# Optimization experiments

Hardware: AMD Instinct MI355X
Metric: run time of the kernel (lower is better)

The kernel has to match this reference:

```python
import jax, jax.numpy as jnp
import numpy as np

METRIC = (1.0, 1.0, 1.0, 1.0, -1.0)  # Cl(4,1) signature
N_HEADS = 8
EPS = 1e-6


def _cayley():
    # Cayley table C[a, b, k]: e_a * e_b = sum_k C[a,b,k] e_k, blades indexed by bitmask over 5 generators.
    C = np.zeros((32, 32, 32), dtype=np.float32)
    for a in range(32):
        for b in range(32):
            s = 0
            t = a >> 1
            while t:
                s += bin(t & b).count('1')
                t >>= 1
            sign = -1.0 if (s & 1) else 1.0
            for i in range(5):
                if (a & b) >> i & 1:
                    sign *= METRIC[i]
            C[a, b, a ^ b] = sign
    return C

_C_NP = _cayley()
GP_MAP = jnp.asarray(_C_NP)  # (32,32,32)
SIG = jnp.asarray(_C_NP[np.arange(32), np.arange(32), 0])  # blade square signs, (32,)


def normalize_cl41(x):
    # normalize each multivector (last-dim 32 blades) to unit RMS
    return x / jnp.sqrt(jnp.mean(x * x, axis=-1, keepdims=True) + EPS)


def versor_linear(x, W):
    # x: (B,S,I,32), W: (O,I,32); out_k = sum_{i,j,l} W[o,i,j] C[j,l,k] x[b,s,i,l]
    O, I, _ = W.shape
    W_op = jnp.einsum('oij,jlk->oilk', W, GP_MAP)  # (O,I,32,32)
    W_mat = W_op.transpose(1, 2, 0, 3).reshape(I * 32, O * 32)
    B, S = x.shape[0], x.shape[1]
    out = (x.reshape(B, S, I * 32) @ W_mat).reshape(B, S, O, 32)
    return normalize_cl41(out)


def versor_attention(x, Wq, Wk, Wv, Wo, lam):
    B, S, D, _ = x.shape
    H = N_HEADS
    hd = D // H

    def split_heads(t):  # (B,S,D,32) -> (B,H,S,hd,32)
        return t.reshape(B, S, H, hd, 32).transpose(0, 2, 1, 3, 4)

    q = split_heads(versor_linear(x, Wq))
    k = split_heads(versor_linear(x, Wk))
    v = split_heads(versor_linear(x, Wv))

    q_flat = (q * SIG).reshape(B, H, S, hd * 32)  # signature-weighted
    k_flat = k.reshape(B, H, S, hd * 32)

    scalar = jnp.einsum('bhsd,bhtd->bhst', q_flat, k_flat)
    scale = 1.0 / jnp.sqrt(jnp.asarray(hd, x.dtype))
    score = scalar * scale

    # torque term: sqrt(relu(|q|^2 |k|^2 - (q.k)^2) + eps) / sqrt(hd)
    q_norm_sq = jnp.sum(q_flat * q_flat, axis=-1)[..., :, None]  # (B,H,S,1)
    k_norm_sq = jnp.sum(k_flat * k_flat, axis=-1)[..., None, :]  # (B,H,1,S)
    torque = jnp.sqrt(jax.nn.relu(q_norm_sq * k_norm_sq - scalar * scalar) + EPS) * scale
    score = score + lam * torque

    probs = jax.nn.softmax(score, axis=-1)
    out = jnp.einsum('bhst,bhtdl->bhsdl', probs, v)  # (B,H,S,hd,32)
    out = out.transpose(0, 2, 1, 3, 4).reshape(B, S, D, 32)
    return versor_linear(out, Wo)


def setup_inputs() -> dict:
    key = jax.random.key(0)
    ks = jax.random.split(key, 5)
    B, S, D = 2, 1024, 128
    std = (2.0 / (D * 32)) ** 0.5  # Versor init
    x = jax.random.normal(ks[0], (B, S, D, 32), jnp.float32)
    Wq = jax.random.normal(ks[1], (D, D, 32), jnp.float32) * std
    Wk = jax.random.normal(ks[2], (D, D, 32), jnp.float32) * std
    Wv = jax.random.normal(ks[3], (D, D, 32), jnp.float32) * std
    Wo = jax.random.normal(ks[4], (D, D, 32), jnp.float32) * std
    attn_lambda = jnp.float32(0.1)
    return {'x': x, 'Wq': Wq, 'Wk': Wk, 'Wv': Wv, 'Wo': Wo, 'attn_lambda': attn_lambda}


def reference(x, Wq, Wk, Wv, Wo, attn_lambda):
    return versor_attention(x, Wq, Wk, Wv, Wo, attn_lambda)
```

## Files before the change

kernel.cpp:

```cpp
#include <hip/hip_runtime.h>
#include <stdint.h>

typedef __attribute__((ext_vector_type(4))) float    f32x4;
typedef __attribute__((ext_vector_type(8))) short    s16x8;
typedef __attribute__((ext_vector_type(4))) short    s16x4;
typedef __attribute__((ext_vector_type(8))) _Float16 f16x8;

#define DEV __device__ __forceinline__

DEV float blade_sign(int a, int b){
    int s = 0, t = a >> 1;
    while (t){ s += __popc(t & b); t >>= 1; }
    float sg = (s & 1) ? -1.0f : 1.0f;
    return ((a & b) & 16) ? -sg : sg;
}
DEV short f2h(float v){
    _Float16 h = (_Float16)v;
    return __builtin_bit_cast(short, h);
}
DEV float h2f(short b){
    return (float)__builtin_bit_cast(_Float16, b);
}
DEV void wait_vm(int n){
    if (n == 8)      asm volatile("s_waitcnt vmcnt(8)" ::: "memory");
    else if (n == 6) asm volatile("s_waitcnt vmcnt(6)" ::: "memory");
    else if (n == 4) asm volatile("s_waitcnt vmcnt(4)" ::: "memory");
    else             asm volatile("s_waitcnt vmcnt(0)" ::: "memory");
}

__global__ __launch_bounds__(256) void cast_f32_f16(const float* __restrict__ in,
                                                    short* __restrict__ out){
    const size_t idx = (size_t)blockIdx.x * 256 + threadIdx.x;
    const float4* p = reinterpret_cast<const float4*>(in) + idx * 2;
    float4 a = p[0], b = p[1];
    s16x8 o;
    o[0]=f2h(a.x); o[1]=f2h(a.y); o[2]=f2h(a.z); o[3]=f2h(a.w);
    o[4]=f2h(b.x); o[5]=f2h(b.y); o[6]=f2h(b.z); o[7]=f2h(b.w);
    *reinterpret_cast<s16x8*>(out + idx * 8) = o;
}

DEV void build_wmat_body(const float* __restrict__ W, short* __restrict__ WmT,
                         int idx){
    const int n  = idx >> 9;
    const int kg = idx & 511;
    const int o = n >> 5, kb = n & 31;
    const int i = kg >> 2, l0 = (kg & 3) * 8;
    const float* wrow = W + (size_t)(o * 128 + i) * 32;
    s16x8 v;
    #pragma unroll
    for (int e = 0; e < 8; ++e){
        const int l = l0 + e, j = kb ^ l;
        v[e] = f2h(wrow[j] * blade_sign(j, l));
    }
    *reinterpret_cast<s16x8*>(WmT + (size_t)n * 4096 + kg * 8) = v;
}

__global__ __launch_bounds__(256) void build_wmat(const float* __restrict__ W,
                                                  short* __restrict__ WmT){
    build_wmat_body(W, WmT, blockIdx.x * 256 + threadIdx.x);
}

__global__ __launch_bounds__(256) void build_wmat3(const float* __restrict__ Wq,
                                                   const float* __restrict__ Wk,
                                                   const float* __restrict__ Wv,
                                                   short* __restrict__ WmT3){
    const int w = blockIdx.y;
    const float* W = (w == 0) ? Wq : ((w == 1) ? Wk : Wv);
    build_wmat_body(W, WmT3 + (size_t)w * 4096 * 4096,
                    blockIdx.x * 256 + threadIdx.x);
}

__global__ __launch_bounds__(256) void row_norms(const short* __restrict__ Q,
                                                 const short* __restrict__ Kq,
                                                 float* __restrict__ Nq,
                                                 float* __restrict__ Nk){
    const int row  = blockIdx.x * 4 + (threadIdx.x >> 6);
    const int lane = threadIdx.x & 63;
    const int b = row >> 13, h = (row >> 10) & 7, s = row & 1023;
    const size_t off = ((size_t)(b * 1024 + s)) * 4096 + h * 512 + lane * 8;
    s16x8 a = *reinterpret_cast<const s16x8*>(Q + off);
    s16x8 c = *reinterpret_cast<const s16x8*>(Kq + off);
    float sq = 0.f, sk = 0.f;
    #pragma unroll
    for (int e = 0; e < 8; ++e){
        float fa = h2f(a[e]); sq = fmaf(fa, fa, sq);
        float fc = h2f(c[e]); sk = fmaf(fc, fc, sk);
    }
    #pragma unroll
    for (int m = 1; m < 64; m <<= 1){
        sq += __shfl_xor(sq, m);
        sk += __shfl_xor(sk, m);
    }
    if (lane == 0){ Nq[row] = sq; Nk[row] = sk; }
}

__global__ __launch_bounds__(256) void softmax_rows(float* __restrict__ Sc){
    const int row  = blockIdx.x * 4 + (threadIdx.x >> 6);
    const int lane = threadIdx.x & 63;
    float* p = Sc + (size_t)row * 1024;
    float v[16];
    float mx = -3.0e38f;
    #pragma unroll
    for (int j = 0; j < 16; ++j){ v[j] = p[lane + j * 64]; mx = fmaxf(mx, v[j]); }
    #pragma unroll
    for (int m = 1; m < 64; m <<= 1) mx = fmaxf(mx, __shfl_xor(mx, m));
    float sum = 0.f;
    #pragma unroll
    for (int j = 0; j < 16; ++j){ v[j] = __expf(v[j] - mx); sum += v[j]; }
    #pragma unroll
    for (int m = 1; m < 64; m <<= 1) sum += __shfl_xor(sum, m);
    const float inv = 1.0f / sum;
    short* pb = reinterpret_cast<short*>(p);
    #pragma unroll
    for (int j = 0; j < 16; ++j) pb[lane + j * 64] = f2h(v[j] * inv);
}

#define GLOAD_LDS(gp, lp) \
    __builtin_amdgcn_global_load_lds( \
        (const __attribute__((address_space(1))) void*)(const void*)(gp), \
        (__attribute__((address_space(3))) void*)(void*)(lp), 16, 0, 0)

#define QKV_STAGE(BUF, T)                                                       \
  {                                                                             \
    const int sb = (BUF) * 12288;                                               \
    GLOAD_LDS(gA0 + (size_t)(T) * 32, lds + sb + dA + 0 * 512);                 \
    GLOAD_LDS(gA1 + (size_t)(T) * 32, lds + sb + dA + 1 * 512);                 \
    GLOAD_LDS(gA2 + (size_t)(T) * 32, lds + sb + dA + 2 * 512);                 \
    GLOAD_LDS(gA3 + (size_t)(T) * 32, lds + sb + dA + 3 * 512);                 \
    GLOAD_LDS(gB0 + (size_t)(T) * 32, lds + sb + dB + 0 * 512);                 \
    GLOAD_LDS(gB1 + (size_t)(T) * 32, lds + sb + dB + 1 * 512);                 \
  }

__global__ __launch_bounds__(256, 3) void versor_gemm_qkv4(
    const short* __restrict__ Xf,
    const short* __restrict__ WmT3,
    short* __restrict__ OQ,
    short* __restrict__ OK,
    short* __restrict__ OV)
{
    __shared__ short lds[2 * 12288];

    const int tid  = threadIdx.x;
    const int lane = tid & 63;
    const int wid  = tid >> 6;
    const int wm   = wid >> 1;
    const int wn   = wid & 1;

    const int wg  = blockIdx.x + blockIdx.y * 96;
    const int xcd = wg & 7;
    const int u   = wg >> 3;
    const int bm  = u & 7;
    const int bn  = xcd * 12 + (u >> 3);
    const int row0 = bm * 256;
    const int col0 = bn * 128;
    const int lda = 4096, ldb = 4096;

    const int jsw = ((lane & 3) ^ ((lane >> 3) & 3)) * 8;
    const short* gA0 = Xf + (size_t)(row0 + wid * 64 + (lane >> 2)) * lda + jsw;
    const short* gA1 = gA0 + (size_t)16 * lda;
    const short* gA2 = gA0 + (size_t)32 * lda;
    const short* gA3 = gA0 + (size_t)48 * lda;
    const short* gB0 = WmT3 + (size_t)(col0 + wid * 32 + (lane >> 2)) * ldb + jsw;
    const short* gB1 = gB0 + (size_t)16 * ldb;
    const int dA = wid * 4 * 512;
    const int dB = 8192 + wid * 2 * 512;

    const int swz = ((lane >> 4) ^ (((lane & 15) >> 1) & 3)) * 8;
    const int ard = (wm * 128 + (lane & 15)) * 32 + swz;
    const int brd = 8192 + (wn * 64 + (lane & 15)) * 32 + swz;

    f32x4 acc[8][4];
    #pragma unroll
    for (int i = 0; i < 8; ++i)
        #pragma unroll
        for (int j = 0; j < 4; ++j)
            acc[i][j] = (f32x4){0.f, 0.f, 0.f, 0.f};

    const int NT = 4096 >> 5;

    QKV_STAGE(0, 0)
    QKV_STAGE(1, 1)

    for (int t = 0; t < NT; ++t){
        if (t + 1 < NT) wait_vm(6);
        else            wait_vm(0);
        __builtin_amdgcn_s_barrier();
        asm volatile("" ::: "memory");
        __builtin_amdgcn_sched_barrier(0);

        const int bb = (t & 1) * 12288;
        f16x8 av[4], bv[4];
        #pragma unroll
        for (int i = 0; i < 4; ++i){
            av[i] = *reinterpret_cast<const f16x8*>(lds + bb + ard + i * 512);
            bv[i] = *reinterpret_cast<const f16x8*>(lds + bb + brd + i * 512);
        }
        __builtin_amdgcn_s_setprio(1);
        #pragma unroll
        for (int mi = 0; mi < 4; ++mi)
            #pragma unroll
            for (int ni = 0; ni < 4; ++ni)
                acc[mi][ni] = __builtin_amdgcn_mfma_f32_16x16x32_f16(
                    av[mi], bv[ni], acc[mi][ni], 0, 0, 0);
        __builtin_amdgcn_s_setprio(0);

        f16x8 aw[4];
        #pragma unroll
        for (int i = 0; i < 4; ++i)
            aw[i] = *reinterpret_cast<const f16x8*>(lds + bb + ard + (4 + i) * 512);
        __builtin_amdgcn_s_setprio(1);
        #pragma unroll
        for (int mi = 0; mi < 4; ++mi)
            #pragma unroll
            for (int ni = 0; ni < 4; ++ni)
                acc[4 + mi][ni] = __builtin_amdgcn_mfma_f32_16x16x32_f16(
                    aw[mi], bv[ni], acc[4 + mi][ni], 0, 0, 0);
        __builtin_amdgcn_s_setprio(0);

        __builtin_amdgcn_s_barrier();
        asm volatile("" ::: "memory");
        __builtin_amdgcn_sched_barrier(0);
        if (t + 2 < NT)
            QKV_STAGE(t & 1, t + 2)
    }

    const int rb = row0 + wm * 128 + (lane >> 4) * 4;

    #pragma unroll
    for (int mi = 0; mi < 8; ++mi){
        #pragma unroll
        for (int g = 0; g < 2; ++g){
            f32x4 a0 = acc[mi][2 * g], a1 = acc[mi][2 * g + 1];
            f32x4 ss = a0 * a0 + a1 * a1;
            #pragma unroll
            for (int m = 1; m < 16; m <<= 1){
                ss.x += __shfl_xor(ss.x, m);
                ss.y += __shfl_xor(ss.y, m);
                ss.z += __shfl_xor(ss.z, m);
                ss.w += __shfl_xor(ss.w, m);
            }
            f32x4 inv;
            inv.x = 1.0f / sqrtf(ss.x * 0.03125f + 1e-6f);
            inv.y = 1.0f / sqrtf(ss.y * 0.03125f + 1e-6f);
            inv.z = 1.0f / sqrtf(ss.z * 0.03125f + 1e-6f);
            inv.w = 1.0f / sqrtf(ss.w * 0.03125f + 1e-6f);
            acc[mi][2 * g]     = a0 * inv;
            acc[mi][2 * g + 1] = a1 * inv;
        }
    }

    const int zsel = col0 >> 12;
    const int cbm  = (col0 & 4095) + wn * 64 + (lane & 15);
    if (zsel == 0){
        const float sg0 = blade_sign(lane & 15, lane & 15);
        const float sg1 = blade_sign(16 | (lane & 15), 16 | (lane & 15));
        #pragma unroll
        for (int mi = 0; mi < 8; ++mi)
            #pragma unroll
            for (int ni = 0; ni < 4; ++ni){
                const f32x4 v = acc[mi][ni] * ((ni & 1) ? sg1 : sg0);
                #pragma unroll
                for (int j = 0; j < 4; ++j)
                    OQ[(size_t)(rb + mi * 16 + j) * 4096 + (cbm + ni * 16)] = f2h(v[j]);
            }
    } else if (zsel == 1){
        #pragma unroll
        for (int mi = 0; mi < 8; ++mi)
            #pragma unroll
            for (int ni = 0; ni < 4; ++ni)
                #pragma unroll
                for (int j = 0; j < 4; ++j)
                    OK[(size_t)(rb + mi * 16 + j) * 4096 + (cbm + ni * 16)] = f2h(acc[mi][ni][j]);
    } else {
        #pragma unroll
        for (int mi = 0; mi < 8; ++mi){
            const int r = rb + mi * 16;
            const int b = r >> 10, tt = r & 1023;
            #pragma unroll
            for (int ni = 0; ni < 4; ++ni){
                const int c = cbm + ni * 16;
                const int h = c >> 9, f = c & 511;
                s16x4 pv;
                #pragma unroll
                for (int j = 0; j < 4; ++j) pv[j] = f2h(acc[mi][ni][j]);
                *reinterpret_cast<s16x4*>(OV + ((size_t)((b * 8 + h) * 512 + f)) * 1024 + tt) = pv;
            }
        }
    }
}

#define R3_TILE(T, WN, PF)                                                      \
  {                                                                             \
    const int bb = cur * 8192;                                                  \
    wait_vm(WN);                                                                \
    __builtin_amdgcn_s_barrier();                                               \
    asm volatile("" ::: "memory");                                              \
    __builtin_amdgcn_sched_barrier(0);                                          \
    const int sb = stg * 8192;                                                  \
    if (PF){                                                                    \
        GLOAD_LDS(gA0 + (size_t)((T) + 2) * 32, lds + sb + dA0);                \
        GLOAD_LDS(gA1 + (size_t)((T) + 2) * 32, lds + sb + dA1);                \
    }                                                                           \
    f16x8 av[4], bv[4];                                                         \
    _Pragma("unroll")                                                           \
    for (int i = 0; i < 4; ++i)                                                 \
        av[i] = *reinterpret_cast<const f16x8*>(lds + bb + ard + i * 512);      \
    bv[0] = *reinterpret_cast<const f16x8*>(lds + bb + brd + 0 * 512);          \
    bv[1] = *reinterpret_cast<const f16x8*>(lds + bb + brd + 1 * 512);          \
    __builtin_amdgcn_s_setprio(1);                                              \
    _Pragma("unroll")                                                           \
    for (int mi = 0; mi < 4; ++mi)                                              \
        _Pragma("unroll")                                                       \
        for (int ni = 0; ni < 2; ++ni)                                          \
            acc[mi][ni] = __builtin_amdgcn_mfma_f32_16x16x32_f16(               \
                av[mi], bv[ni], acc[mi][ni], 0, 0, 0);                          \
    __builtin_amdgcn_s_setprio(0);                                              \
    if (PF){                                                                    \
        GLOAD_LDS(gB0 + (size_t)((T) + 2) * 32, lds + sb + dB0);                \
        GLOAD_LDS(gB1 + (size_t)((T) + 2) * 32, lds + sb + dB1);                \
    }                                                                           \
    bv[2] = *reinterpret_cast<const f16x8*>(lds + bb + brd + 2 * 512);          \
    bv[3] = *reinterpret_cast<const f16x8*>(lds + bb + brd + 3 * 512);          \
    __builtin_amdgcn_s_setprio(1);                                              \
    _Pragma("unroll")                                                           \
    for (int mi = 0; mi < 4; ++mi)                                              \
        _Pragma("unroll")                                                       \
        for (int ni = 2; ni < 4; ++ni)                                          \
            acc[mi][ni] = __builtin_amdgcn_mfma_f32_16x16x32_f16(               \
                av[mi], bv[ni], acc[mi][ni], 0, 0, 0);                          \
    __builtin_amdgcn_s_setprio(0);                                              \
    cur = (cur == 2) ? 0 : cur + 1;                                             \
    stg = (stg == 2) ? 0 : stg + 1;                                             \
  }

template<int EPI, int CPX>
__global__ __launch_bounds__(256, 3) void versor_gemm_r3(
    const short* __restrict__ Abase, int lda,
    const short* __restrict__ Bbase, int ldb,
    int K, void* __restrict__ OutP)
{
    __shared__ short lds[3 * 8192];

    const int tid  = threadIdx.x;
    const int lane = tid & 63;
    const int wid  = tid >> 6;
    const int wr   = wid >> 1;
    const int wc   = wid & 1;
    const int z    = blockIdx.z;

    int bn, bm;
    if constexpr (CPX > 0){
        const int wg  = blockIdx.x + blockIdx.y * gridDim.x;
        const int xcd = wg & 7;
        const int u   = wg >> 3;
        bm = u & 15;
        bn = xcd * CPX + (u >> 4);
    } else {
        bn = blockIdx.x; bm = blockIdx.y;
    }

    const short* A = Abase;
    const short* B = Bbase;
    if constexpr (EPI == 5){
        A += (size_t)z * 1024 * 2048;
        B += (size_t)z * 512 * 1024;
    }
    const int row0 = bm * 128;
    const int col0 = bn * 128;

    const int jsw = ((lane & 3) ^ ((lane >> 3) & 3)) * 8;
    const short* gA0 = A + (size_t)(row0 + wid * 16 + (lane >> 2)) * lda + jsw;
    const short* gA1 = gA0 + (size_t)64 * lda;
    const short* gB0 = B + (size_t)(col0 + wid * 16 + (lane >> 2)) * ldb + jsw;
    const short* gB1 = gB0 + (size_t)64 * ldb;
    const int dA0 = wid * 512,        dA1 = 2048 + wid * 512;
    const int dB0 = 4096 + wid * 512, dB1 = 6144 + wid * 512;

    const int swz = ((lane >> 4) ^ (((lane & 15) >> 1) & 3)) * 8;
    const int ard = (wr * 64 + (lane & 15)) * 32 + swz;
    const int brd = 4096 + (wc * 64 + (lane & 15)) * 32 + swz;

    f32x4 acc[4][4];
    #pragma unroll
    for (int i = 0; i < 4; ++i)
        #pragma unroll
        for (int j = 0; j < 4; ++j)
            acc[i][j] = (f32x4){0.f, 0.f, 0.f, 0.f};

    const int NT = K >> 5;

    #pragma unroll
    for (int pt = 0; pt < 2; ++pt){
        const int sb = pt * 8192;
        GLOAD_LDS(gA0 + pt * 32, lds + sb + dA0);
        GLOAD_LDS(gA1 + pt * 32, lds + sb + dA1);
        GLOAD_LDS(gB0 + pt * 32, lds + sb + dB0);
        GLOAD_LDS(gB1 + pt * 32, lds + sb + dB1);
    }

    int cur = 0, stg = 2;
    for (int t = 0; t < NT - 1; ++t)
        R3_TILE(t, 4, (t + 2 < NT))
    R3_TILE(NT - 1, 0, false)

    const int rb = row0 + wr * 64 + (lane >> 4) * 4;
    const int cb = col0 + wc * 64 + (lane & 15);

    if constexpr (EPI == 3){
        #pragma unroll
        for (int mi = 0; mi < 4; ++mi){
            #pragma unroll
            for (int g = 0; g < 2; ++g){
                f32x4 a0 = acc[mi][2 * g], a1 = acc[mi][2 * g + 1];
                f32x4 ss = a0 * a0 + a1 * a1;
                #pragma unroll
                for (int m = 1; m < 16; m <<= 1){
                    ss.x += __shfl_xor(ss.x, m);
                    ss.y += __shfl_xor(ss.y, m);
                    ss.z += __shfl_xor(ss.z, m);
                    ss.w += __shfl_xor(ss.w, m);
                }
                f32x4 inv;
                inv.x = 1.0f / sqrtf(ss.x * 0.03125f + 1e-6f);
                inv.y = 1.0f / sqrtf(ss.y * 0.03125f + 1e-6f);
                inv.z = 1.0f / sqrtf(ss.z * 0.03125f + 1e-6f);
                inv.w = 1.0f / sqrtf(ss.w * 0.03125f + 1e-6f);
                acc[mi][2 * g]     = a0 * inv;
                acc[mi][2 * g + 1] = a1 * inv;
            }
        }
        float* Of = (float*)OutP;
        #pragma unroll
        for (int mi = 0; mi < 4; ++mi)
            #pragma unroll
            for (int ni = 0; ni < 4; ++ni)
                #pragma unroll
                for (int j = 0; j < 4; ++j)
                    Of[(size_t)(rb + mi * 16 + j) * 4096 + (cb + ni * 16)] = acc[mi][ni][j];
    }
    if constexpr (EPI == 5){
        short* Ob = (short*)OutP;
        const int b = z >> 3, h = z & 7;
        #pragma unroll
        for (int mi = 0; mi < 4; ++mi)
            #pragma unroll
            for (int ni = 0; ni < 4; ++ni)
                #pragma unroll
                for (int j = 0; j < 4; ++j)
                    Ob[(size_t)(b * 1024 + rb + mi * 16 + j) * 4096 + h * 512 + (cb + ni * 16)]
                        = f2h(acc[mi][ni][j]);
    }
}

#define SC_TILE(T, WN, PF)                                                      \
  {                                                                             \
    const int bb = ((T) & 3) * 16384;                                           \
    wait_vm(WN);                                                                \
    __builtin_amdgcn_s_barrier();                                               \
    asm volatile("" ::: "memory");                                              \
    __builtin_amdgcn_sched_barrier(0);                                          \
    if (PF){                                                                    \
        const int nb = (((T) + 3) & 3) * 16384;                                 \
        GLOAD_LDS(gA0 + (size_t)((T) + 3) * 32, lds + nb + dA0);                \
        GLOAD_LDS(gA1 + (size_t)((T) + 3) * 32, lds + nb + dA1);                \
    }                                                                           \
    f16x8 av[4], bv[4];                                                         \
    _Pragma("unroll")                                                           \
    for (int i = 0; i < 4; ++i){                                                \
        av[i] = *reinterpret_cast<const f16x8*>(lds + bb + ard + i * 512);      \
        bv[i] = *reinterpret_cast<const f16x8*>(lds + bb + brd + i * 512);      \
    }                                                                           \
    __builtin_amdgcn_s_setprio(1);                                              \
    _Pragma("unroll")                                                           \
    for (int mi = 0; mi < 4; ++mi)                                              \
        _Pragma("unroll")                                                       \
        for (int ni = 0; ni < 4; ++ni)                                          \
            acc[mi][ni] = __builtin_amdgcn_mfma_f32_16x16x32_f16(               \
                av[mi], bv[ni], acc[mi][ni], 0, 0, 0);                          \
    __builtin_amdgcn_s_setprio(0);                                              \
    if (PF){                                                                    \
        const int nb = (((T) + 3) & 3) * 16384;                                 \
        GLOAD_LDS(gB0 + (size_t)((T) + 3) * 32, lds + nb + dB0);                \
        GLOAD_LDS(gB1 + (size_t)((T) + 3) * 32, lds + nb + dB1);                \
    }                                                                           \
    f16x8 aw[4];                                                                \
    _Pragma("unroll")                                                           \
    for (int i = 0; i < 4; ++i)                                                 \
        aw[i] = *reinterpret_cast<const f16x8*>(lds + bb + ard + (4 + i) * 512);\
    __builtin_amdgcn_s_setprio(1);                                              \
    _Pragma("unroll")                                                           \
    for (int mi = 0; mi < 4; ++mi)                                              \
        _Pragma("unroll")                                                       \
        for (int ni = 0; ni < 4; ++ni)                                          \
            acc[4 + mi][ni] = __builtin_amdgcn_mfma_f32_16x16x32_f16(           \
                aw[mi], bv[ni], acc[4 + mi][ni], 0, 0, 0);                      \
    __builtin_amdgcn_s_setprio(0);                                              \
  }

__global__ __launch_bounds__(512, 2) void versor_gemm_sc(
    const short* __restrict__ Qbase, const short* __restrict__ Kbase,
    int K, float* __restrict__ OutP,
    const float* __restrict__ NqP, const float* __restrict__ NkP,
    const float* __restrict__ LamP)
{
    extern __shared__ short lds[];

    const int tid  = threadIdx.x;
    const int lane = tid & 63;
    const int wid  = tid >> 6;
    const int wm   = wid >> 2;
    const int wn   = wid & 3;
    const int z    = blockIdx.z;

    const int b = z >> 3, h = z & 7;
    const size_t off = (size_t)b * 1024 * 4096 + (size_t)h * 512;
    const short* A = Qbase + off;
    const short* B = Kbase + off;
    const int lda = 4096, ldb = 4096;
    const int row0 = blockIdx.y * 256;
    const int col0 = blockIdx.x * 256;

    const int jsw = ((lane & 3) ^ ((lane >> 3) & 3)) * 8;
    const short* gA0 = A + (size_t)(row0 + wid * 32 + (lane >> 2)) * lda + jsw;
    const short* gA1 = gA0 + (size_t)16 * lda;
    const short* gB0 = B + (size_t)(col0 + wid * 32 + (lane >> 2)) * ldb + jsw;
    const short* gB1 = gB0 + (size_t)16 * ldb;
    const int dA0 = wid * 1024, dA1 = dA0 + 512;
    const int dB0 = 8192 + wid * 1024, dB1 = dB0 + 512;

    const int swz = ((lane >> 4) ^ (((lane & 15) >> 1) & 3)) * 8;
    const int ard = (wm * 128 + (lane & 15)) * 32 + swz;
    const int brd = 8192 + (wn * 64 + (lane & 15)) * 32 + swz;

    f32x4 acc[8][4];
    #pragma unroll
    for (int i = 0; i < 8; ++i)
        #pragma unroll
        for (int j = 0; j < 4; ++j)
            acc[i][j] = (f32x4){0.f, 0.f, 0.f, 0.f};

    const int NT = K >> 5;

    #pragma unroll
    for (int pt = 0; pt < 3; ++pt){
        const int bb = pt * 16384;
        GLOAD_LDS(gA0 + pt * 32, lds + bb + dA0);
        GLOAD_LDS(gA1 + pt * 32, lds + bb + dA1);
        GLOAD_LDS(gB0 + pt * 32, lds + bb + dB0);
        GLOAD_LDS(gB1 + pt * 32, lds + bb + dB1);
    }

    for (int t = 0; t < NT - 2; ++t)
        SC_TILE(t, 8, (t + 3 < NT))
    SC_TILE(NT - 2, 4, false)
    SC_TILE(NT - 1, 0, false)

    const int rb = row0 + wm * 128 + (lane >> 4) * 4;
    const int cb = col0 + wn * 64 + (lane & 15);

    float* Of = OutP + (size_t)z * 1024 * 1024;
    const float lam = *LamP;
    const float* nq = NqP + z * 1024;
    const float* nk = NkP + z * 1024;
    #pragma unroll
    for (int mi = 0; mi < 8; ++mi)
        #pragma unroll
        for (int j = 0; j < 4; ++j){
            const int r = rb + mi * 16 + j;
            const float qn = nq[r];
            #pragma unroll
            for (int ni = 0; ni < 4; ++ni){
                const int c = cb + ni * 16;
                const float sc = acc[mi][ni][j];
                const float tq = sqrtf(fmaxf(qn * nk[c] - sc * sc, 0.0f) + 1e-6f);
                Of[(size_t)r * 1024 + c] = 0.25f * (sc + lam * tq);
            }
        }
}

extern "C" void kernel_launch(void* const* d_in, const int* in_sizes, int n_in,
                              void* d_out, int out_size, void* d_ws, size_t ws_size,
                              hipStream_t stream)
{
    (void)in_sizes; (void)n_in; (void)out_size; (void)ws_size;
    const float* x   = (const float*)d_in[0];
    const float* Wq  = (const float*)d_in[1];
    const float* Wk  = (const float*)d_in[2];
    const float* Wv  = (const float*)d_in[3];
    const float* Wo  = (const float*)d_in[4];
    const float* lam = (const float*)d_in[5];
    float* out = (float*)d_out;
    char*  ws  = (char*)d_ws;

    short* Xf   = (short*)(ws);
    short* WmT3 = (short*)(ws + (16u  << 20));
    short* Qf   = (short*)(ws + (112u << 20));
    short* Kf   = (short*)(ws + (128u << 20));
    short* Vt   = (short*)(ws + (144u << 20));
    float* Nq   = (float*)(ws + (160u << 20));
    float* Nk   = (float*)(ws + (160u << 20) + (64u << 10));
    float* Sc   = (float*)(ws + (16u  << 20));
    short* WmTo = (short*)(ws + (80u  << 20));
    short* Attn = Xf;

    const int SC_LDS = 131072;
    hipFuncSetAttribute(reinterpret_cast<const void*>(versor_gemm_sc),
                        hipFuncAttributeMaxDynamicSharedMemorySize, SC_LDS);

    dim3 blk(256), blk8(512);
    cast_f32_f16<<<4096, blk, 0, stream>>>(x, Xf);

    dim3 gw3(8192, 3);
    build_wmat3<<<gw3, blk, 0, stream>>>(Wq, Wk, Wv, WmT3);

    dim3 gqkv(96, 8, 1);
    versor_gemm_qkv4<<<gqkv, blk, 0, stream>>>(Xf, WmT3, Qf, Kf, Vt);

    row_norms<<<4096, blk, 0, stream>>>(Qf, Kf, Nq, Nk);

    build_wmat<<<8192, blk, 0, stream>>>(Wo, WmTo);

    dim3 gsc(4, 4, 16);
    versor_gemm_sc<<<gsc, blk8, SC_LDS, stream>>>(Qf, Kf, 512, Sc, Nq, Nk, lam);
    softmax_rows<<<4096, blk, 0, stream>>>(Sc);

    dim3 gpv(4, 8, 16);
    versor_gemm_r3<5, 0><<<gpv, blk, 0, stream>>>(
        (const short*)Sc, 2048, Vt, 1024, 1024, Attn);

    dim3 gfin(32, 16, 1);
    versor_gemm_r3<3, 4><<<gfin, blk, 0, stream>>>(
        Attn, 4096, WmTo, 4096, 4096, out);
}
```

Baseline: 528.5 us.

## Restructure QKV GEMM into 256x256 tiles with 8 waves and interleaved prefetch

Replaces the 256x128-tile, 4-wave QKV projection GEMM with a 256x256-tile, 8-wave kernel that uses 128 KB of dynamic LDS and a K-step of 64 split into two halves. Global-to-LDS prefetch of the next tile is spread across the MFMA phases with extra barriers, aiming for more operand reuse per loaded byte and better overlap of loads with math. The cost is one workgroup per CU (384 workgroups), more barriers per iteration, and less latency hiding from co-resident blocks.

```diff
diff --git a/kernel.cpp b/kernel.cpp
--- a/kernel.cpp
+++ b/kernel.cpp
@@ -120,54 +120,58 @@
         (const __attribute__((address_space(1))) void*)(const void*)(gp), \
         (__attribute__((address_space(3))) void*)(void*)(lp), 16, 0, 0)
 
-#define QKV_STAGE(BUF, T)                                                       \
-  {                                                                             \
-    const int sb = (BUF) * 12288;                                               \
-    GLOAD_LDS(gA0 + (size_t)(T) * 32, lds + sb + dA + 0 * 512);                 \
-    GLOAD_LDS(gA1 + (size_t)(T) * 32, lds + sb + dA + 1 * 512);                 \
-    GLOAD_LDS(gA2 + (size_t)(T) * 32, lds + sb + dA + 2 * 512);                 \
-    GLOAD_LDS(gA3 + (size_t)(T) * 32, lds + sb + dA + 3 * 512);                 \
-    GLOAD_LDS(gB0 + (size_t)(T) * 32, lds + sb + dB + 0 * 512);                 \
-    GLOAD_LDS(gB1 + (size_t)(T) * 32, lds + sb + dB + 1 * 512);                 \
-  }
-
-__global__ __launch_bounds__(256, 3) void versor_gemm_qkv4(
+#define Q7_ST_A(BUF, T, H)                                                      \
+  { short* d = lds + (BUF) * 32768 + (H) * 8192 + wid * 1024;                   \
+    const short* s = gA + (size_t)(T) * 64 + (H) * 32;                          \
+    GLOAD_LDS(s, d);                                                            \
+    GLOAD_LDS(s + (size_t)16 * 4096, d + 512); }
+
+#define Q7_ST_B(BUF, T, H)                                                      \
+  { short* d = lds + (BUF) * 32768 + 16384 + (H) * 8192 + wid * 1024;           \
+    const short* s = gB + (size_t)(T) * 64 + (H) * 32;                          \
+    GLOAD_LDS(s, d);                                                            \
+    GLOAD_LDS(s + (size_t)16 * 4096, d + 512); }
+
+#define Q7_MFMA8(MBASE, BK)                                                     \
+    __builtin_amdgcn_s_setprio(1);                                              \
+    _Pragma("unroll")                                                           \
+    for (int mi = 0; mi < 4; ++mi)                                              \
+        _Pragma("unroll")                                                       \
+        for (int ni = 0; ni < 4; ++ni)                                          \
+            acc[(MBASE) + mi][ni] = __builtin_amdgcn_mfma_f32_16x16x32_f16(     \
+                a[mi], BK[ni], acc[(MBASE) + mi][ni], 0, 0, 0);                 \
+    __builtin_amdgcn_s_setprio(0);
+
+__global__ __launch_bounds__(512, 1) void versor_gemm_qkv7(
     const short* __restrict__ Xf,
     const short* __restrict__ WmT3,
     short* __restrict__ OQ,
     short* __restrict__ OK,
     short* __restrict__ OV)
 {
-    __shared__ short lds[2 * 12288];
+    extern __shared__ short lds[];
 
     const int tid  = threadIdx.x;
     const int lane = tid & 63;
     const int wid  = tid >> 6;
-    const int wm   = wid >> 1;
-    const int wn   = wid & 1;
-
-    const int wg  = blockIdx.x + blockIdx.y * 96;
+    const int wm   = wid >> 2;
+    const int wn   = wid & 3;
+
+    const int wg  = blockIdx.x + blockIdx.y * 48;
     const int xcd = wg & 7;
     const int u   = wg >> 3;
     const int bm  = u & 7;
-    const int bn  = xcd * 12 + (u >> 3);
+    const int bn  = xcd * 6 + (u >> 3);
     const int row0 = bm * 256;
-    const int col0 = bn * 128;
-    const int lda = 4096, ldb = 4096;
+    const int col0 = bn * 256;
 
     const int jsw = ((lane & 3) ^ ((lane >> 3) & 3)) * 8;
-    const short* gA0 = Xf + (size_t)(row0 + wid * 64 + (lane >> 2)) * lda + jsw;
-    const short* gA1 = gA0 + (size_t)16 * lda;
-    const short* gA2 = gA0 + (size_t)32 * lda;
-    const short* gA3 = gA0 + (size_t)48 * lda;
-    const short* gB0 = WmT3 + (size_t)(col0 + wid * 32 + (lane >> 2)) * ldb + jsw;
-    const short* gB1 = gB0 + (size_t)16 * ldb;
-    const int dA = wid * 4 * 512;
-    const int dB = 8192 + wid * 2 * 512;
+    const short* gA = Xf   + (size_t)(row0 + wid * 32 + (lane >> 2)) * 4096 + jsw;
+    const short* gB = WmT3 + (size_t)(col0 + wid * 32 + (lane >> 2)) * 4096 + jsw;
 
     const int swz = ((lane >> 4) ^ (((lane & 15) >> 1) & 3)) * 8;
     const int ard = (wm * 128 + (lane & 15)) * 32 + swz;
-    const int brd = 8192 + (wn * 64 + (lane & 15)) * 32 + swz;
+    const int brd = (wn * 64 + (lane & 15)) * 32 + swz;
 
     f32x4 acc[8][4];
     #pragma unroll
@@ -176,52 +180,61 @@
         for (int j = 0; j < 4; ++j)
             acc[i][j] = (f32x4){0.f, 0.f, 0.f, 0.f};
 
-    const int NT = 4096 >> 5;
-
-    QKV_STAGE(0, 0)
-    QKV_STAGE(1, 1)
+    const int NT = 64;
+
+    Q7_ST_A(0, 0, 0)
+    Q7_ST_B(0, 0, 0)
+    Q7_ST_A(0, 0, 1)
+    Q7_ST_B(0, 0, 1)
 
     for (int t = 0; t < NT; ++t){
-        if (t + 1 < NT) wait_vm(6);
-        else            wait_vm(0);
+        const int bb = (t & 1) * 32768;
+        const int nbuf = (t + 1) & 1;
+        const bool pf = (t + 1 < NT);
+        f16x8 a[4], bk0[4], bk1[4];
+
+        wait_vm(4);
         __builtin_amdgcn_s_barrier();
         asm volatile("" ::: "memory");
         __builtin_amdgcn_sched_barrier(0);
-
-        const int bb = (t & 1) * 12288;
-        f16x8 av[4], bv[4];
-        #pragma unroll
-        for (int i = 0; i < 4; ++i){
-            av[i] = *reinterpret_cast<const f16x8*>(lds + bb + ard + i * 512);
-            bv[i] = *reinterpret_cast<const f16x8*>(lds + bb + brd + i * 512);
-        }
-        __builtin_amdgcn_s_setprio(1);
+        #pragma unroll
+        for (int ni = 0; ni < 4; ++ni)
+            bk0[ni] = *reinterpret_cast<const f16x8*>(lds + bb + 16384 + brd + ni * 512);
         #pragma unroll
         for (int mi = 0; mi < 4; ++mi)
-            #pragma unroll
-            for (int ni = 0; ni < 4; ++ni)
-                acc[mi][ni] = __builtin_amdgcn_mfma_f32_16x16x32_f16(
-                    av[mi], bv[ni], acc[mi][ni], 0, 0, 0);
-        __builtin_amdgcn_s_setprio(0);
-
-        f16x8 aw[4];
-        #pragma unroll
-        for (int i = 0; i < 4; ++i)
-            aw[i] = *reinterpret_cast<const f16x8*>(lds + bb + ard + (4 + i) * 512);
-        __builtin_amdgcn_s_setprio(1);
+            a[mi] = *reinterpret_cast<const f16x8*>(lds + bb + ard + mi * 512);
+        if (pf) Q7_ST_A(nbuf, t + 1, 0)
+        __builtin_amdgcn_s_barrier();
+        Q7_MFMA8(0, bk0)
+
         #pragma unroll
         for (int mi = 0; mi < 4; ++mi)
-            #pragma unroll
-            for (int ni = 0; ni < 4; ++ni)
-                acc[4 + mi][ni] = __builtin_amdgcn_mfma_f32_16x16x32_f16(
-                    aw[mi], bv[ni], acc[4 + mi][ni], 0, 0, 0);
-        __builtin_amdgcn_s_setprio(0);
-
+            a[mi] = *reinterpret_cast<const f16x8*>(lds + bb + ard + (4 + mi) * 512);
+        if (pf) Q7_ST_B(nbuf, t + 1, 0)
+        __builtin_amdgcn_s_barrier();
+        Q7_MFMA8(4, bk0)
+
+        if (pf) wait_vm(4);
+        else    wait_vm(0);
         __builtin_amdgcn_s_barrier();
         asm volatile("" ::: "memory");
         __builtin_amdgcn_sched_barrier(0);
-        if (t + 2 < NT)
-            QKV_STAGE(t & 1, t + 2)
+        #pragma unroll
+        for (int ni = 0; ni < 4; ++ni)
+            bk1[ni] = *reinterpret_cast<const f16x8*>(lds + bb + 24576 + brd + ni * 512);
+        #pragma unroll
+        for (int mi = 0; mi < 4; ++mi)
+            a[mi] = *reinterpret_cast<const f16x8*>(lds + bb + 8192 + ard + mi * 512);
+        if (pf) Q7_ST_A(nbuf, t + 1, 1)
+        __builtin_amdgcn_s_barrier();
+        Q7_MFMA8(0, bk1)
+
+        #pragma unroll
+        for (int mi = 0; mi < 4; ++mi)
+            a[mi] = *reinterpret_cast<const f16x8*>(lds + bb + 8192 + ard + (4 + mi) * 512);
+        if (pf) Q7_ST_B(nbuf, t + 1, 1)
+        __builtin_amdgcn_s_barrier();
+        Q7_MFMA8(4, bk1)
     }
 
     const int rb = row0 + wm * 128 + (lane >> 4) * 4;
@@ -603,9 +616,12 @@
     short* WmTo = (short*)(ws + (80u  << 20));
     short* Attn = Xf;
 
-    const int SC_LDS = 131072;
+    const int SC_LDS  = 131072;
+    const int Q7_LDS  = 131072;
     hipFuncSetAttribute(reinterpret_cast<const void*>(versor_gemm_sc),
                         hipFuncAttributeMaxDynamicSharedMemorySize, SC_LDS);
+    hipFuncSetAttribute(reinterpret_cast<const void*>(versor_gemm_qkv7),
+                        hipFuncAttributeMaxDynamicSharedMemorySize, Q7_LDS);
 
     dim3 blk(256), blk8(512);
     cast_f32_f16<<<4096, blk, 0, stream>>>(x, Xf);
@@ -613,8 +629,8 @@
     dim3 gw3(8192, 3);
     build_wmat3<<<gw3, blk, 0, stream>>>(Wq, Wk, Wv, WmT3);
 
-    dim3 gqkv(96, 8, 1);
-    versor_gemm_qkv4<<<gqkv, blk, 0, stream>>>(Xf, WmT3, Qf, Kf, Vt);
+    dim3 gqkv(48, 8, 1);
+    versor_gemm_qkv7<<<gqkv, blk8, Q7_LDS, stream>>>(Xf, WmT3, Qf, Kf, Vt);
 
     row_norms<<<4096, blk, 0, stream>>>(Qf, Kf, Nq, Nk);
 
```

After: 535.2 us. About the same (+1.3%).
